# Optimization experiments

Hardware: AMD Instinct MI355X
Metric: run time of the kernel (lower is better)

Reference implementation:

```python
import jax, jax.numpy as jnp
import numpy as np

V, D, B, C, NEG = 100000, 512, 1024, 20, 64


def setup_inputs() -> dict:
    key = jax.random.key(0)
    k1, k2, k3, k4, k5 = jax.random.split(key, 5)
    center_ids = jax.random.randint(k1, (B,), 0, V)
    context_ids = jax.random.randint(k2, (B, C), 0, V)
    W_center = jax.random.normal(k3, (V, D), dtype=jnp.float32)
    W_context = jax.random.normal(k4, (V, D), dtype=jnp.float32)
    freq = jax.random.uniform(k5, (V,), dtype=jnp.float32, minval=1e-4, maxval=1.0)
    p = freq ** 0.75
    sample_prob = p / p.sum()
    return {
        "center_ids": center_ids,
        "context_ids": context_ids,
        "W_center": W_center,
        "W_context": W_context,
        "sample_prob": sample_prob,
        "neg_sample": NEG,
    }


def _sample_negatives(sample_prob, batch, neg):
    # Gumbel top-k == sampling `neg` items without replacement w.p. proportional to sample_prob.
    log_p = jnp.log(sample_prob)  # [V]
    g = jax.random.gumbel(jax.random.key(42), (batch, sample_prob.shape[0]), dtype=sample_prob.dtype)
    _, idx = jax.lax.top_k(log_p[None, :] + g, neg)  # [B, neg]
    return idx


def reference(center_ids, context_ids, W_center, W_context, sample_prob, neg_sample):
    b, c = context_ids.shape
    embs_center = W_center[center_ids]                    # [B, D]
    # NOTE: original module looks up positive context in the CENTER table (faithful quirk).
    embs_context = W_center[context_ids]                  # [B, C, D]
    neg_idx = _sample_negatives(sample_prob, b, neg_sample)
    embs_negatives = W_context[neg_idx]                   # [B, neg, D]
    cos_positive = jnp.einsum('bcd,bd->bc', embs_context, embs_center)[..., None]   # [B, C, 1]
    cos_negative = jnp.einsum('bnd,bd->bn', embs_negatives, embs_center)[..., None]  # [B, neg, 1]
    return cos_positive, cos_negative
```

## Files before the change

### kernel.cpp

```cpp
#include <hip/hip_runtime.h>
#include <stdint.h>
#include <math.h>

#define V_SZ 100000
#define D_SZ 512
#define B_SZ 1024
#define C_SZ 20
#define NEG 64
#define NB 2048
#define CAP 512
#define TCUT -5.5451774f

__device__ __forceinline__ float xla_logf(float xin) {
#pragma clang fp contract(off)
  float x = fmaxf(xin, 1.17549435e-38f);
  uint32_t bits = __float_as_uint(x);
  float e = (float)((int)(bits >> 23) - 127) + 1.0f;
  float m = __uint_as_float((bits & 0x807fffffu) | 0x3f000000u);
  bool lt = m < 0.707106781186547524f;
  float tmp = lt ? m : 0.0f;
  m = m - 1.0f;
  e = e - (lt ? 1.0f : 0.0f);
  m = m + tmp;
  float z = m * m;
  float y = 7.0376836292E-2f;
  y = fmaf(y, m, -1.1514610310E-1f);
  y = fmaf(y, m, 1.1676998740E-1f);
  y = fmaf(y, m, -1.2420140846E-1f);
  y = fmaf(y, m, 1.4249322787E-1f);
  y = fmaf(y, m, -1.6668057665E-1f);
  y = fmaf(y, m, 2.0000714765E-1f);
  y = fmaf(y, m, -2.4999993993E-1f);
  y = fmaf(y, m, 3.3333331174E-1f);
  y = y * m;
  y = y * z;
  y = y + e * (-2.12194440e-4f);
  y = y - z * 0.5f;
  x = m + y;
  x = x + e * 0.693359375f;
  return x;
}

__device__ __forceinline__ void threefry2x32(uint32_t x0, uint32_t x1,
                                             uint32_t& o0, uint32_t& o1) {
  const uint32_t ks1 = 42u, ks2 = 0x1BD11BF0u;
#define TFR(r) { x0 += x1; x1 = (x1 << (r)) | (x1 >> (32 - (r))); x1 ^= x0; }
  x0 += 0u; x1 += ks1;
  TFR(13) TFR(15) TFR(26) TFR(6)
  x0 += ks1; x1 += ks2 + 1u;
  TFR(17) TFR(29) TFR(16) TFR(24)
  x0 += ks2; x1 += 0u + 2u;
  TFR(13) TFR(15) TFR(26) TFR(6)
  x0 += 0u; x1 += ks1 + 3u;
  TFR(17) TFR(29) TFR(16) TFR(24)
  x0 += ks1; x1 += ks2 + 4u;
  TFR(13) TFR(15) TFR(26) TFR(6)
  x0 += ks2; x1 += 0u + 5u;
#undef TFR
  o0 = x0; o1 = x1;
}

__device__ __forceinline__ uint32_t tf_bits_partitionable(uint32_t i) {
  uint32_t o0, o1;
  threefry2x32(0u, i, o0, o1);
  return o0 ^ o1;
}

__device__ __forceinline__ float gumbel_from_bits(uint32_t bits) {
#pragma clang fp contract(off)
  float f = __uint_as_float((bits >> 9) | 0x3f800000u) - 1.0f;
  float u = (bits >> 9) ? f : 1.17549435e-38f;
  return -xla_logf(-xla_logf(u));
}

__device__ __forceinline__ float score_one(uint32_t i, float lpv) {
#pragma clang fp contract(off)
  return lpv + gumbel_from_bits(tf_bits_partitionable(i));
}

__global__ __launch_bounds__(256) void compute_thr(const float* __restrict__ sp,
                                                   uint32_t* __restrict__ thr) {
  int v = blockIdx.x * 256 + threadIdx.x;
  if (v >= V_SZ) return;
  float lpv = xla_logf(sp[v]);
  float need = TCUT - lpv;
  float u = expf(-expf(-need));
  int m = (int)floorf(u * 8388608.0f) - 128;
  thr[v] = (uint32_t)(m < 0 ? 0 : m);
}

__global__ __launch_bounds__(256) void select_negs(const float* __restrict__ sp,
                                                   const uint32_t* __restrict__ thr,
                                                   int* __restrict__ negidx) {
  __shared__ uint32_t hist[NB];
  __shared__ float cs[CAP];
  __shared__ int   ci[CAP];
  __shared__ int   cnt;
  __shared__ int   cnt_hi;
  __shared__ int   cut;

  const int b = blockIdx.x;
  const uint32_t base = (uint32_t)b * (uint32_t)V_SZ;

  if (threadIdx.x == 0) { cnt = 0; cnt_hi = 0; }
  __syncthreads();

  for (int v = threadIdx.x; v < V_SZ; v += 256) {
    uint32_t bits = tf_bits_partitionable(base + (uint32_t)v);
    if ((bits >> 9) >= thr[v]) {
      float s = xla_logf(sp[v]) + gumbel_from_bits(bits);
      int k = atomicAdd(&cnt, 1);
      if (k < CAP) { cs[k] = s; ci[k] = v; }
      if (s >= TCUT) atomicAdd(&cnt_hi, 1);
    }
  }
  __syncthreads();

  if (cnt <= CAP && cnt_hi >= NEG) {
    int n = cnt;
    for (int i = threadIdx.x; i < n; i += 256) {
      float si = cs[i]; int vi = ci[i];
      int rank = 0;
      for (int j = 0; j < n; ++j) {
        float sj = cs[j];
        rank += (sj > si) || (sj == si && ci[j] < vi);
      }
      if (rank < NEG) negidx[b * NEG + rank] = vi;
    }
    return;
  }

  const float LO = -28.0f, INVW = 51.2f;
  for (int i = threadIdx.x; i < NB; i += 256) hist[i] = 0u;
  if (threadIdx.x == 0) cnt = 0;
  __syncthreads();

  for (int v = threadIdx.x; v < V_SZ; v += 256) {
    float s = score_one(base + (uint32_t)v, xla_logf(sp[v]));
    int bin = min(NB - 1, max(0, (int)((s - LO) * INVW)));
    atomicAdd(&hist[bin], 1u);
  }
  __syncthreads();

  if (threadIdx.x == 0) {
    uint32_t acc = 0; int c = NB - 1;
    for (; c > 0; --c) { acc += hist[c]; if (acc >= (uint32_t)NEG) break; }
    cut = c;
  }
  __syncthreads();
  const int cutb = cut;

  for (int v = threadIdx.x; v < V_SZ; v += 256) {
    float s = score_one(base + (uint32_t)v, xla_logf(sp[v]));
    int bin = min(NB - 1, max(0, (int)((s - LO) * INVW)));
    if (bin >= cutb) {
      int k = atomicAdd(&cnt, 1);
      if (k < CAP) { cs[k] = s; ci[k] = v; }
    }
  }
  __syncthreads();

  int n = min(cnt, CAP);
  for (int i = threadIdx.x; i < n; i += 256) {
    float si = cs[i]; int vi = ci[i];
    int rank = 0;
    for (int j = 0; j < n; ++j) {
      float sj = cs[j];
      rank += (sj > si) || (sj == si && ci[j] < vi);
    }
    if (rank < NEG) negidx[b * NEG + rank] = vi;
  }
}

__global__ __launch_bounds__(256) void dots(const int* __restrict__ center_ids,
                                            const int* __restrict__ context_ids,
                                            const float* __restrict__ Wcen,
                                            const float* __restrict__ Wctx,
                                            const int* __restrict__ negidx,
                                            float* __restrict__ out) {
  __shared__ float cen[D_SZ];
  const int b = blockIdx.x;
  const int cid = center_ids[b];
  const float4* crow = (const float4*)(Wcen + (size_t)cid * D_SZ);
  for (int i = threadIdx.x; i < D_SZ / 4; i += 256) ((float4*)cen)[i] = crow[i];
  __syncthreads();

  const int wave = threadIdx.x >> 6, lane = threadIdx.x & 63;
  const float4 c0 = ((const float4*)cen)[lane * 2];
  const float4 c1 = ((const float4*)cen)[lane * 2 + 1];

  for (int it0 = wave; it0 < C_SZ + NEG; it0 += 16) {
    float4 a0[4], a1[4];
#pragma unroll
    for (int u = 0; u < 4; ++u) {
      int item = it0 + 4 * u;
      if (item < C_SZ + NEG) {
        const float* row;
        if (item < C_SZ) row = Wcen + (size_t)context_ids[b * C_SZ + item] * D_SZ;
        else             row = Wctx + (size_t)negidx[b * NEG + (item - C_SZ)] * D_SZ;
        const float4* r4 = (const float4*)row;
        a0[u] = r4[lane * 2];
        a1[u] = r4[lane * 2 + 1];
      }
    }
#pragma unroll
    for (int u = 0; u < 4; ++u) {
      int item = it0 + 4 * u;
      if (item < C_SZ + NEG) {
        float p = a0[u].x * c0.x + a0[u].y * c0.y + a0[u].z * c0.z + a0[u].w * c0.w +
                  a1[u].x * c1.x + a1[u].y * c1.y + a1[u].z * c1.z + a1[u].w * c1.w;
        for (int off = 32; off; off >>= 1) p += __shfl_xor(p, off, 64);
        if (lane == 0) {
          if (item < C_SZ) out[b * C_SZ + item] = p;
          else out[B_SZ * C_SZ + b * NEG + (item - C_SZ)] = p;
        }
      }
    }
  }
}

extern "C" void kernel_launch(void* const* d_in, const int* in_sizes, int n_in,
                              void* d_out, int out_size, void* d_ws, size_t ws_size,
                              hipStream_t stream) {
  (void)in_sizes; (void)n_in; (void)out_size; (void)ws_size;
  const int*   center_ids  = (const int*)d_in[0];
  const int*   context_ids = (const int*)d_in[1];
  const float* Wcen        = (const float*)d_in[2];
  const float* Wctx        = (const float*)d_in[3];
  const float* sp          = (const float*)d_in[4];

  uint32_t* thr    = (uint32_t*)d_ws;
  int*      negidx = (int*)((char*)d_ws + 512 * 1024);

  compute_thr<<<(V_SZ + 255) / 256, 256, 0, stream>>>(sp, thr);
  select_negs<<<B_SZ,              256, 0, stream>>>(sp, thr, negidx);
  dots       <<<B_SZ,              256, 0, stream>>>(center_ids, context_ids,
                                                     Wcen, Wctx, negidx,
                                                     (float*)d_out);
}
```

Before: 693.1 us.

## Defer gumbel scoring of candidates, prescale thresholds, and flatten dot kernel to one wave per item

The selection scan now compares raw threefry bits against a threshold pre-shifted by 9, so no shift is needed per element. It stores only candidate index and bits during the scan, and computes log and gumbel scores in a second pass over the few candidates. Moving the transcendental work out of the divergent hot loop is meant to cut per-thread cost in the 100k-element scan. The rotate is written as a builtin, the scan loop is unrolled by 2, and the dot-product kernel is rewritten to map one wave to each (batch, item) pair, which gives more parallelism but reloads the center row for every item.

```diff
diff --git a/kernel.cpp b/kernel.cpp
--- a/kernel.cpp
+++ b/kernel.cpp
@@ -9,6 +9,7 @@
 #define NEG 64
 #define NB 2048
 #define CAP 512
+#define ITEMS (C_SZ + NEG)
 #define TCUT -5.5451774f
 
 __device__ __forceinline__ float xla_logf(float xin) {
@@ -44,7 +45,7 @@
 __device__ __forceinline__ void threefry2x32(uint32_t x0, uint32_t x1,
                                              uint32_t& o0, uint32_t& o1) {
   const uint32_t ks1 = 42u, ks2 = 0x1BD11BF0u;
-#define TFR(r) { x0 += x1; x1 = (x1 << (r)) | (x1 >> (32 - (r))); x1 ^= x0; }
+#define TFR(r) { x0 += x1; x1 = __builtin_rotateleft32(x1, (r)); x1 ^= x0; }
   x0 += 0u; x1 += ks1;
   TFR(13) TFR(15) TFR(26) TFR(6)
   x0 += ks1; x1 += ks2 + 1u;
@@ -79,25 +80,26 @@
 }
 
 __global__ __launch_bounds__(256) void compute_thr(const float* __restrict__ sp,
-                                                   uint32_t* __restrict__ thr) {
+                                                   uint32_t* __restrict__ thr_pre) {
   int v = blockIdx.x * 256 + threadIdx.x;
   if (v >= V_SZ) return;
   float lpv = xla_logf(sp[v]);
   float need = TCUT - lpv;
   float u = expf(-expf(-need));
   int m = (int)floorf(u * 8388608.0f) - 128;
-  thr[v] = (uint32_t)(m < 0 ? 0 : m);
+  thr_pre[v] = ((uint32_t)(m < 0 ? 0 : m)) << 9;
 }
 
 __global__ __launch_bounds__(256) void select_negs(const float* __restrict__ sp,
-                                                   const uint32_t* __restrict__ thr,
+                                                   const uint32_t* __restrict__ thr_pre,
                                                    int* __restrict__ negidx) {
   __shared__ uint32_t hist[NB];
-  __shared__ float cs[CAP];
-  __shared__ int   ci[CAP];
-  __shared__ int   cnt;
-  __shared__ int   cnt_hi;
-  __shared__ int   cut;
+  __shared__ float    cs[CAP];
+  __shared__ int      ci[CAP];
+  __shared__ uint32_t cb[CAP];
+  __shared__ int      cnt;
+  __shared__ int      cnt_hi;
+  __shared__ int      cut;
 
   const int b = blockIdx.x;
   const uint32_t base = (uint32_t)b * (uint32_t)V_SZ;
@@ -105,14 +107,21 @@
   if (threadIdx.x == 0) { cnt = 0; cnt_hi = 0; }
   __syncthreads();
 
+#pragma unroll 2
   for (int v = threadIdx.x; v < V_SZ; v += 256) {
     uint32_t bits = tf_bits_partitionable(base + (uint32_t)v);
-    if ((bits >> 9) >= thr[v]) {
-      float s = xla_logf(sp[v]) + gumbel_from_bits(bits);
+    if (bits >= thr_pre[v]) {
       int k = atomicAdd(&cnt, 1);
-      if (k < CAP) { cs[k] = s; ci[k] = v; }
-      if (s >= TCUT) atomicAdd(&cnt_hi, 1);
-    }
+      if (k < CAP) { ci[k] = v; cb[k] = bits; }
+    }
+  }
+  __syncthreads();
+
+  int n0 = min(cnt, CAP);
+  for (int i = threadIdx.x; i < n0; i += 256) {
+    float s = xla_logf(sp[ci[i]]) + gumbel_from_bits(cb[i]);
+    cs[i] = s;
+    if (s >= TCUT) atomicAdd(&cnt_hi, 1);
   }
   __syncthreads();
 
@@ -178,44 +187,29 @@
                                             const float* __restrict__ Wctx,
                                             const int* __restrict__ negidx,
                                             float* __restrict__ out) {
-  __shared__ float cen[D_SZ];
-  const int b = blockIdx.x;
-  const int cid = center_ids[b];
-  const float4* crow = (const float4*)(Wcen + (size_t)cid * D_SZ);
-  for (int i = threadIdx.x; i < D_SZ / 4; i += 256) ((float4*)cen)[i] = crow[i];
-  __syncthreads();
-
-  const int wave = threadIdx.x >> 6, lane = threadIdx.x & 63;
-  const float4 c0 = ((const float4*)cen)[lane * 2];
-  const float4 c1 = ((const float4*)cen)[lane * 2 + 1];
-
-  for (int it0 = wave; it0 < C_SZ + NEG; it0 += 16) {
-    float4 a0[4], a1[4];
-#pragma unroll
-    for (int u = 0; u < 4; ++u) {
-      int item = it0 + 4 * u;
-      if (item < C_SZ + NEG) {
-        const float* row;
-        if (item < C_SZ) row = Wcen + (size_t)context_ids[b * C_SZ + item] * D_SZ;
-        else             row = Wctx + (size_t)negidx[b * NEG + (item - C_SZ)] * D_SZ;
-        const float4* r4 = (const float4*)row;
-        a0[u] = r4[lane * 2];
-        a1[u] = r4[lane * 2 + 1];
-      }
-    }
-#pragma unroll
-    for (int u = 0; u < 4; ++u) {
-      int item = it0 + 4 * u;
-      if (item < C_SZ + NEG) {
-        float p = a0[u].x * c0.x + a0[u].y * c0.y + a0[u].z * c0.z + a0[u].w * c0.w +
-                  a1[u].x * c1.x + a1[u].y * c1.y + a1[u].z * c1.z + a1[u].w * c1.w;
-        for (int off = 32; off; off >>= 1) p += __shfl_xor(p, off, 64);
-        if (lane == 0) {
-          if (item < C_SZ) out[b * C_SZ + item] = p;
-          else out[B_SZ * C_SZ + b * NEG + (item - C_SZ)] = p;
-        }
-      }
-    }
+  const int wid  = blockIdx.x * 4 + (threadIdx.x >> 6);
+  const int lane = threadIdx.x & 63;
+  const int b = wid / ITEMS;
+  const int j = wid - b * ITEMS;
+
+  const float4* crow = (const float4*)(Wcen + (size_t)center_ids[b] * D_SZ);
+  const float* row;
+  if (j < C_SZ) row = Wcen + (size_t)context_ids[b * C_SZ + j] * D_SZ;
+  else          row = Wctx + (size_t)negidx[b * NEG + (j - C_SZ)] * D_SZ;
+  const float4* r4 = (const float4*)row;
+
+  float4 a0 = r4[lane * 2];
+  float4 a1 = r4[lane * 2 + 1];
+  float4 c0 = crow[lane * 2];
+  float4 c1 = crow[lane * 2 + 1];
+
+  float p = a0.x * c0.x + a0.y * c0.y + a0.z * c0.z + a0.w * c0.w +
+            a1.x * c1.x + a1.y * c1.y + a1.z * c1.z + a1.w * c1.w;
+  for (int off = 32; off; off >>= 1) p += __shfl_xor(p, off, 64);
+
+  if (lane == 0) {
+    if (j < C_SZ) out[b * C_SZ + j] = p;
+    else          out[B_SZ * C_SZ + b * NEG + (j - C_SZ)] = p;
   }
 }
 
@@ -229,12 +223,12 @@
   const float* Wctx        = (const float*)d_in[3];
   const float* sp          = (const float*)d_in[4];
 
-  uint32_t* thr    = (uint32_t*)d_ws;
-  int*      negidx = (int*)((char*)d_ws + 512 * 1024);
-
-  compute_thr<<<(V_SZ + 255) / 256, 256, 0, stream>>>(sp, thr);
-  select_negs<<<B_SZ,              256, 0, stream>>>(sp, thr, negidx);
-  dots       <<<B_SZ,              256, 0, stream>>>(center_ids, context_ids,
-                                                     Wcen, Wctx, negidx,
-                                                     (float*)d_out);
-}
+  uint32_t* thr_pre = (uint32_t*)d_ws;
+  int*      negidx  = (int*)((char*)d_ws + 512 * 1024);
+
+  compute_thr<<<(V_SZ + 255) / 256, 256, 0, stream>>>(sp, thr_pre);
+  select_negs<<<B_SZ,              256, 0, stream>>>(sp, thr_pre, negidx);
+  dots       <<<(B_SZ * ITEMS) / 4, 256, 0, stream>>>(center_ids, context_ids,
+                                                      Wcen, Wctx, negidx,
+                                                      (float*)d_out);
+}
```

After: 654.9 us. 1.06x faster.
